# Kernel tuning notes

Hardware: AMD Instinct MI355X
Metric: run time of the kernel (lower is better)

The kernel has to match this reference:

```python
import jax, jax.numpy as jnp
import numpy as np

NUM_HEADS = 12
EMBED_DIM = 768
HEAD_DIM = EMBED_DIM // NUM_HEADS


def _rope_cos_sin():
    # Faithful to source: RoPE is applied with seq_dim=1 on [b,h,n,d] tensors,
    # so the "position" axis is actually the HEAD axis (length NUM_HEADS).
    inv_freq = 1.0 / (10000.0 ** (jnp.arange(0, HEAD_DIM, 2, dtype=jnp.float32) / HEAD_DIM))
    t = jnp.arange(NUM_HEADS, dtype=jnp.float32)
    freqs = t[:, None] * inv_freq[None, :]            # [H, D/2]
    emb = jnp.concatenate([freqs, freqs], axis=-1)     # [H, D]
    cos = jnp.cos(emb)[None, :, None, :]               # [1, H, 1, D] broadcasts over seq
    sin = jnp.sin(emb)[None, :, None, :]
    return cos, sin


def _apply_rope(x, cos, sin):
    # x: [B, H, N, D]
    x1, x2 = jnp.split(x, 2, axis=-1)
    x_rot = jnp.concatenate([-x2, x1], axis=-1)
    return x * cos + x_rot * sin


def setup_inputs() -> dict:
    key = jax.random.key(0)
    k1, k2, k3, k4, k5 = jax.random.split(key, 5)
    B, N, E = 8, 1024, EMBED_DIM
    s_in = 1.0 / np.sqrt(E)
    return {
        "x": jax.random.normal(k1, (B, N, E), dtype=jnp.float32),
        "w_qkv": jax.random.uniform(k2, (E, 3 * E), dtype=jnp.float32, minval=-s_in, maxval=s_in),
        "b_qkv": jax.random.uniform(k3, (3 * E,), dtype=jnp.float32, minval=-s_in, maxval=s_in),
        "w_proj": jax.random.uniform(k4, (E, E), dtype=jnp.float32, minval=-s_in, maxval=s_in),
        "b_proj": jax.random.uniform(k5, (E,), dtype=jnp.float32, minval=-s_in, maxval=s_in),
    }


def reference(x, w_qkv, b_qkv, w_proj, b_proj):
    B, N, E = x.shape
    H, D = NUM_HEADS, HEAD_DIM
    scale = D ** (-0.5)

    qkv = x @ w_qkv + b_qkv                                  # [B, N, 3E]
    qkv = qkv.reshape(B, N, 3, H, D).transpose(2, 0, 3, 1, 4)  # [3, B, H, N, D]
    q, k, v = qkv[0], qkv[1], qkv[2]

    cos, sin = _rope_cos_sin()
    q = _apply_rope(q, cos, sin)
    k = _apply_rope(k, cos, sin)

    attn = jnp.einsum('bhid,bhjd->bhij', q, k) * scale       # [B, H, N, N]
    attn = jax.nn.softmax(attn, axis=-1)
    out = jnp.einsum('bhij,bhjd->bhid', attn, v)             # [B, H, N, D]
    out = out.transpose(0, 2, 1, 3).reshape(B, N, E)         # [B, N, E]
    return out @ w_proj + b_proj
```

## Files before the change

kernel.cpp:

```cpp
#include <hip/hip_runtime.h>
#include <math.h>

#define NH 12
#define HD 64
#define NSEQ 1024
#define BATCH 8
#define EMB 768
#define NQKV 2304
#define MROWS 8192

typedef _Float16 half8 __attribute__((ext_vector_type(8)));
typedef _Float16 half4 __attribute__((ext_vector_type(4)));
typedef _Float16 half2v __attribute__((ext_vector_type(2)));
typedef float f32x4 __attribute__((ext_vector_type(4)));
typedef float f32x16 __attribute__((ext_vector_type(16)));
typedef unsigned int u32;

#define MFMA16(a,b,c) __builtin_amdgcn_mfma_f32_16x16x32_f16(a, b, c, 0, 0, 0)
#define MFMA32(a,b,c) __builtin_amdgcn_mfma_f32_32x32x16_f16(a, b, c, 0, 0, 0)

__device__ __forceinline__ void gld_lds16(const _Float16* g, _Float16* l) {
  __builtin_amdgcn_global_load_lds((const __attribute__((address_space(1))) u32*)g,
                                   (__attribute__((address_space(3))) u32*)l, 16, 0, 0);
}

__device__ __forceinline__ void transpose_tile(const float* __restrict__ in,
                                               _Float16* __restrict__ out,
                                               int R, int C, int bx, int by,
                                               _Float16 (*T)[72]) {
  const int tr = by * 64, tc = bx * 64;
  const int r = threadIdx.x >> 2, s = threadIdx.x & 3;
  const float* src = in + (size_t)(tr + r) * C + tc + s * 16;
  _Float16* dst = &T[r][s * 16];
  #pragma unroll
  for (int i = 0; i < 4; ++i) {
    float4 v = ((const float4*)src)[i];
    dst[4*i+0] = (_Float16)v.x; dst[4*i+1] = (_Float16)v.y;
    dst[4*i+2] = (_Float16)v.z; dst[4*i+3] = (_Float16)v.w;
  }
  __syncthreads();
  alignas(16) _Float16 tmp[16];
  #pragma unroll
  for (int j = 0; j < 16; ++j) tmp[j] = T[s * 16 + j][r];
  half8* o = (half8*)(out + (size_t)(tc + r) * R + tr + s * 16);
  o[0] = *(half8*)&tmp[0];
  o[1] = *(half8*)&tmp[8];
}

__global__ __launch_bounds__(256) void prepass(const float* __restrict__ x,
                                               _Float16* __restrict__ xh,
                                               const float* __restrict__ wq,
                                               _Float16* __restrict__ wqT,
                                               const float* __restrict__ wp,
                                               _Float16* __restrict__ wpT) {
  __shared__ _Float16 T[64][72];
  const int bid = blockIdx.x;
  if (bid < 6144) {
    int i = bid * 256 + threadIdx.x;
    float4 v = ((const float4*)x)[i];
    half4 h = { (_Float16)v.x, (_Float16)v.y, (_Float16)v.z, (_Float16)v.w };
    ((half4*)xh)[i] = h;
  } else if (bid < 6576) {
    int idx = bid - 6144;
    transpose_tile(wq, wqT, EMB, NQKV, idx % 36, idx / 36, T);
  } else {
    int idx = bid - 6576;
    transpose_tile(wp, wpT, EMB, EMB, idx % 12, idx / 12, T);
  }
}

template<int MODE>
__global__ __launch_bounds__(256) void gemm_mfma(const _Float16* __restrict__ A,
                                                 const _Float16* __restrict__ BT,
                                                 const float* __restrict__ bias,
                                                 float* __restrict__ outf,
                                                 _Float16* __restrict__ qo,
                                                 _Float16* __restrict__ ko,
                                                 _Float16* __restrict__ vo,
                                                 int K) {
  const int BUFH = 128 * 32;
  __shared__ __align__(16) _Float16 As[2 * 128 * 32];
  __shared__ __align__(16) _Float16 Bs[2 * 128 * 32];
  const int tid = threadIdx.x;
  const int lane = tid & 63, wave = tid >> 6;
  const int quad = lane >> 4, l15 = lane & 15;
  const int wm = (wave >> 1) * 64, wn = (wave & 1) * 64;
  const int row0 = blockIdx.y * 128, col0 = blockIdx.x * 128;

  const int srow = lane >> 2;
  const int sseg = (lane & 3) ^ ((srow >> 1) & 3);
  const _Float16* gA = A + (size_t)(row0 + wave*32 + srow) * K + sseg * 8;
  const _Float16* gB = BT + (size_t)(col0 + wave*32 + srow) * K + sseg * 8;
  _Float16* lA0 = As + (wave*32) * 32;
  _Float16* lA1 = As + (wave*32 + 16) * 32;
  _Float16* lB0 = Bs + (wave*32) * 32;
  _Float16* lB1 = Bs + (wave*32 + 16) * 32;

  const int xq = (quad ^ ((l15 >> 1) & 3)) * 8;

  f32x4 acc[4][4];
  #pragma unroll
  for (int i = 0; i < 4; ++i)
    #pragma unroll
    for (int j = 0; j < 4; ++j) {
      f32x4 z = {0.f, 0.f, 0.f, 0.f};
      acc[i][j] = z;
    }

  gld_lds16(gA,          lA0);
  gld_lds16(gA + 16 * K, lA1);
  gld_lds16(gB,          lB0);
  gld_lds16(gB + 16 * K, lB1);

  int buf = 0;
  for (int k0 = 0; k0 < K; k0 += 32, buf ^= 1) {
    __syncthreads();
    if (k0 + 32 < K) {
      const int nb = (buf ^ 1) * BUFH;
      gld_lds16(gA + k0 + 32,          lA0 + nb);
      gld_lds16(gA + k0 + 32 + 16 * K, lA1 + nb);
      gld_lds16(gB + k0 + 32,          lB0 + nb);
      gld_lds16(gB + k0 + 32 + 16 * K, lB1 + nb);
    }
    const _Float16* Ab = As + buf * BUFH;
    const _Float16* Bb = Bs + buf * BUFH;
    half8 af[4], bf[4];
    #pragma unroll
    for (int mt = 0; mt < 4; ++mt)
      af[mt] = *(const half8*)(Ab + (wm + mt*16 + l15) * 32 + xq);
    #pragma unroll
    for (int nt = 0; nt < 4; ++nt)
      bf[nt] = *(const half8*)(Bb + (wn + nt*16 + l15) * 32 + xq);
    #pragma unroll
    for (int mt = 0; mt < 4; ++mt)
      #pragma unroll
      for (int nt = 0; nt < 4; ++nt)
        acc[mt][nt] = MFMA16(af[mt], bf[nt], acc[mt][nt]);
  }

  float bcol[4];
  #pragma unroll
  for (int nt = 0; nt < 4; ++nt)
    bcol[nt] = bias[col0 + wn + nt*16 + l15];

  if (MODE == 0) {
    const int ch = col0 + wn;
    const int tt = ch / EMB;
    const int hh = (ch % EMB) >> 6;
    float cs[2], sn[2];
    if (tt < 2) {
      #pragma unroll
      for (int j = 0; j < 2; ++j) {
        float fi = (float)(j*16 + l15);
        float ang = (float)hh * expf(-0.28782313662425574f * fi);
        sincosf(ang, &sn[j], &cs[j]);
      }
    }
    #pragma unroll
    for (int mt = 0; mt < 4; ++mt) {
      int m0 = row0 + wm + mt*16 + quad*4;
      int b = m0 >> 10, n0 = m0 & 1023;
      size_t bh = (size_t)(b * NH + hh);
      if (tt == 2) {
        int np = (n0 & ~12) | ((n0 & 4) << 1) | ((n0 & 8) >> 1);
        #pragma unroll
        for (int nt = 0; nt < 4; ++nt) {
          int d = nt*16 + l15;
          half4 pk;
          #pragma unroll
          for (int r = 0; r < 4; ++r)
            pk[r] = (_Float16)(acc[mt][nt][r] + bcol[nt]);
          *(half4*)(vo + (bh * HD + d) * NSEQ + np) = pk;
        }
      } else {
        _Float16* dst = (tt == 0) ? qo : ko;
        const float sc = (tt == 0) ? 0.125f : 1.0f;
        #pragma unroll
        for (int j = 0; j < 2; ++j) {
          #pragma unroll
          for (int r = 0; r < 4; ++r) {
            float lo = acc[mt][j][r]     + bcol[j];
            float hi = acc[mt][j + 2][r] + bcol[j + 2];
            float nlo = (lo * cs[j] - hi * sn[j]) * sc;
            float nhi = (hi * cs[j] + lo * sn[j]) * sc;
            size_t rowoff = (bh * NSEQ + (size_t)(n0 + r)) * HD;
            dst[rowoff + j*16 + l15]      = (_Float16)nlo;
            dst[rowoff + j*16 + l15 + 32] = (_Float16)nhi;
          }
        }
      }
    }
  } else {
    #pragma unroll
    for (int mt = 0; mt < 4; ++mt) {
      int m0 = row0 + wm + mt*16 + quad*4;
      #pragma unroll
      for (int nt = 0; nt < 4; ++nt)
        #pragma unroll
        for (int r = 0; r < 4; ++r)
          outf[(size_t)(m0 + r) * EMB + col0 + wn + nt*16 + l15] =
              acc[mt][nt][r] + bcol[nt];
    }
  }
}

__global__ __launch_bounds__(256) void attn_mfma32(const _Float16* __restrict__ q,
                                                   const _Float16* __restrict__ k,
                                                   const _Float16* __restrict__ vt,
                                                   _Float16* __restrict__ ao) {
  const int BUFH = 64 * 64;
  __shared__ __align__(16) _Float16 Ks[2 * 64 * 64];
  __shared__ __align__(16) _Float16 Vs[2 * 64 * 64];
  const int tid = threadIdx.x;
  const int lane = tid & 63, wave = tid >> 6;
  const int l31 = lane & 31, hi = lane >> 5;
  const int bh = blockIdx.y;
  const int qrow = blockIdx.x * 128 + wave * 32 + l31;
  const size_t base = (size_t)bh * NSEQ * HD;

  const _Float16* qp = q + base + (size_t)qrow * HD + hi * 8;
  half8 qf[4];
  #pragma unroll
  for (int kh = 0; kh < 4; ++kh)
    qf[kh] = *(const half8*)(qp + kh * 16);

  const int srow = lane >> 3;
  const int sxor = (lane & 7) ^ (srow & 7);
  const _Float16* kg = k + base + (size_t)(wave*16 + srow) * HD + sxor * 8;
  const _Float16* vg = vt + (size_t)bh * HD * NSEQ
                       + (size_t)(wave*16 + srow) * NSEQ + sxor * 8;
  const int lofs = (wave * 16) * 64;

  int xofs[4];
  #pragma unroll
  for (int kh = 0; kh < 4; ++kh)
    xofs[kh] = ((kh*2 + hi) ^ (l31 & 7)) * 8;

  f32x16 O[2];
  #pragma unroll
  for (int dt = 0; dt < 2; ++dt)
    #pragma unroll
    for (int r = 0; r < 16; ++r) O[dt][r] = 0.f;
  float l = 0.f;

  gld_lds16(kg,             Ks + lofs);
  gld_lds16(kg + 8 * HD,    Ks + lofs + 8 * 64);
  gld_lds16(vg,             Vs + lofs);
  gld_lds16(vg + 8 * NSEQ,  Vs + lofs + 8 * 64);

  int buf = 0;
  for (int c0 = 0; c0 < NSEQ; c0 += 64, buf ^= 1) {
    __syncthreads();
    if (c0 + 64 < NSEQ) {
      const int nb = (buf ^ 1) * BUFH;
      gld_lds16(kg + (size_t)(c0 + 64) * HD,      Ks + nb + lofs);
      gld_lds16(kg + (size_t)(c0 + 72) * HD,      Ks + nb + lofs + 8 * 64);
      gld_lds16(vg + c0 + 64,                     Vs + nb + lofs);
      gld_lds16(vg + 8 * NSEQ + c0 + 64,          Vs + nb + lofs + 8 * 64);
    }
    const _Float16* Kb = Ks + buf * BUFH;
    const _Float16* Vb = Vs + buf * BUFH;

    f32x16 ct[2];
    #pragma unroll
    for (int kt = 0; kt < 2; ++kt) {
      #pragma unroll
      for (int r = 0; r < 16; ++r) ct[kt][r] = 0.f;
      #pragma unroll
      for (int kh = 0; kh < 4; ++kh) {
        half8 kf = *(const half8*)(Kb + (kt*32 + l31) * 64 + xofs[kh]);
        ct[kt] = MFMA32(kf, qf[kh], ct[kt]);
      }
    }

    union { half2v v; int i; } ph2[16];
    float rs = 0.f;
    #pragma unroll
    for (int kt = 0; kt < 2; ++kt)
      #pragma unroll
      for (int rp = 0; rp < 8; ++rp) {
        float p0 = __expf(ct[kt][2*rp]     - 4.0f);
        float p1 = __expf(ct[kt][2*rp + 1] - 4.0f);
        rs += p0 + p1;
        half2v hp = { (_Float16)p0, (_Float16)p1 };
        ph2[kt*8 + rp].v = hp;
      }
    l += rs;

    #pragma unroll
    for (int kh = 0; kh < 4; ++kh) {
      const int kt = kh >> 1;
      const int iA = kt*8 + (kh & 1)*4;
      union { half8 h; int d[4]; } pf;
      pf.d[0] = ph2[iA].i;     pf.d[1] = ph2[iA + 1].i;
      pf.d[2] = ph2[iA + 2].i; pf.d[3] = ph2[iA + 3].i;
      #pragma unroll
      for (int dt = 0; dt < 2; ++dt) {
        half8 vf = *(const half8*)(Vb + (dt*32 + l31) * 64 + xofs[kh]);
        O[dt] = MFMA32(vf, pf.h, O[dt]);
      }
    }
  }

  l += __shfl_xor(l, 32);

  const int b = bh / NH, hh = bh % NH;
  const float inv = 1.0f / l;
  _Float16* orow = ao + (size_t)(b * NSEQ + qrow) * EMB + hh * HD;
  #pragma unroll
  for (int dt = 0; dt < 2; ++dt)
    #pragma unroll
    for (int t = 0; t < 4; ++t) {
      int d0 = dt*32 + 8*t + 4*hi;
      half4 o4;
      #pragma unroll
      for (int j = 0; j < 4; ++j)
        o4[j] = (_Float16)(O[dt][4*t + j] * inv);
      *(half4*)(orow + d0) = o4;
    }
}

extern "C" void kernel_launch(void* const* d_in, const int* in_sizes, int n_in,
                              void* d_out, int out_size, void* d_ws, size_t ws_size,
                              hipStream_t stream) {
  const float* x      = (const float*)d_in[0];
  const float* w_qkv  = (const float*)d_in[1];
  const float* b_qkv  = (const float*)d_in[2];
  const float* w_proj = (const float*)d_in[3];
  const float* b_proj = (const float*)d_in[4];
  float* out = (float*)d_out;

  _Float16* xh  = (_Float16*)d_ws;
  _Float16* wqT = xh  + (size_t)MROWS * EMB;
  _Float16* wpT = wqT + (size_t)NQKV * EMB;
  _Float16* qh  = wpT + (size_t)EMB * EMB;
  _Float16* kh  = qh  + (size_t)BATCH*NH*NSEQ*HD;
  _Float16* vth = kh  + (size_t)BATCH*NH*NSEQ*HD;
  _Float16* aoh = vth + (size_t)BATCH*NH*NSEQ*HD;

  prepass<<<6720, 256, 0, stream>>>(x, xh, w_qkv, wqT, w_proj, wpT);

  gemm_mfma<0><<<dim3(NQKV/128, MROWS/128), 256, 0, stream>>>(
      xh, wqT, b_qkv, nullptr, qh, kh, vth, EMB);

  attn_mfma32<<<dim3(NSEQ/128, BATCH*NH), 256, 0, stream>>>(qh, kh, vth, aoh);

  gemm_mfma<1><<<dim3(EMB/128, MROWS/128), 256, 0, stream>>>(
      aoh, wpT, b_proj, out, nullptr, nullptr, nullptr, EMB);
}
```

Measured before the change: 205.7 us.

## Replace direct global-to-LDS loads with register-staged double-buffered prefetch

Both the GEMM and the attention kernel stop using global_load_lds and instead load the next tile into registers at the start of each iteration, compute on the current LDS buffer, then write the registers into the other LDS buffer before one barrier. The swizzle moves from the global address to the LDS write address. The aim is to hide global latency behind the MFMA work and to move the barrier to the end of the loop. In exchange it adds VGPR pressure and separate ds_write instructions, which can lower occupancy.

Measured after the change: 201.9 us. About the same (-1.9%).

```diff
diff --git a/kernel.cpp b/kernel.cpp
--- a/kernel.cpp
+++ b/kernel.cpp
@@ -18,11 +18,6 @@
 
 #define MFMA16(a,b,c) __builtin_amdgcn_mfma_f32_16x16x32_f16(a, b, c, 0, 0, 0)
 #define MFMA32(a,b,c) __builtin_amdgcn_mfma_f32_32x32x16_f16(a, b, c, 0, 0, 0)
-
-__device__ __forceinline__ void gld_lds16(const _Float16* g, _Float16* l) {
-  __builtin_amdgcn_global_load_lds((const __attribute__((address_space(1))) u32*)g,
-                                   (__attribute__((address_space(3))) u32*)l, 16, 0, 0);
-}
 
 __device__ __forceinline__ void transpose_tile(const float* __restrict__ in,
                                                _Float16* __restrict__ out,
@@ -88,13 +83,12 @@
   const int row0 = blockIdx.y * 128, col0 = blockIdx.x * 128;
 
   const int srow = lane >> 2;
-  const int sseg = (lane & 3) ^ ((srow >> 1) & 3);
+  const int sseg = lane & 3;
+  const int wseg = sseg ^ ((srow >> 1) & 3);
   const _Float16* gA = A + (size_t)(row0 + wave*32 + srow) * K + sseg * 8;
   const _Float16* gB = BT + (size_t)(col0 + wave*32 + srow) * K + sseg * 8;
-  _Float16* lA0 = As + (wave*32) * 32;
-  _Float16* lA1 = As + (wave*32 + 16) * 32;
-  _Float16* lB0 = Bs + (wave*32) * 32;
-  _Float16* lB1 = Bs + (wave*32 + 16) * 32;
+  _Float16* wA0 = As + (wave*32 + srow) * 32 + wseg * 8;
+  _Float16* wB0 = Bs + (wave*32 + srow) * 32 + wseg * 8;
 
   const int xq = (quad ^ ((l15 >> 1) & 3)) * 8;
 
@@ -107,20 +101,24 @@
       acc[i][j] = z;
     }
 
-  gld_lds16(gA,          lA0);
-  gld_lds16(gA + 16 * K, lA1);
-  gld_lds16(gB,          lB0);
-  gld_lds16(gB + 16 * K, lB1);
+  half8 ra0 = *(const half8*)(gA);
+  half8 ra1 = *(const half8*)(gA + 16 * K);
+  half8 rb0 = *(const half8*)(gB);
+  half8 rb1 = *(const half8*)(gB + 16 * K);
+  *(half8*)(wA0)          = ra0;
+  *(half8*)(wA0 + 16*32)  = ra1;
+  *(half8*)(wB0)          = rb0;
+  *(half8*)(wB0 + 16*32)  = rb1;
+  __syncthreads();
 
   int buf = 0;
-  for (int k0 = 0; k0 < K; k0 += 32, buf ^= 1) {
-    __syncthreads();
-    if (k0 + 32 < K) {
-      const int nb = (buf ^ 1) * BUFH;
-      gld_lds16(gA + k0 + 32,          lA0 + nb);
-      gld_lds16(gA + k0 + 32 + 16 * K, lA1 + nb);
-      gld_lds16(gB + k0 + 32,          lB0 + nb);
-      gld_lds16(gB + k0 + 32 + 16 * K, lB1 + nb);
+  for (int k0 = 0; k0 < K; k0 += 32) {
+    const bool more = (k0 + 32 < K);
+    if (more) {
+      ra0 = *(const half8*)(gA + k0 + 32);
+      ra1 = *(const half8*)(gA + k0 + 32 + 16 * K);
+      rb0 = *(const half8*)(gB + k0 + 32);
+      rb1 = *(const half8*)(gB + k0 + 32 + 16 * K);
     }
     const _Float16* Ab = As + buf * BUFH;
     const _Float16* Bb = Bs + buf * BUFH;
@@ -136,6 +134,15 @@
       #pragma unroll
       for (int nt = 0; nt < 4; ++nt)
         acc[mt][nt] = MFMA16(af[mt], bf[nt], acc[mt][nt]);
+    if (more) {
+      const int nb = (buf ^ 1) * BUFH;
+      *(half8*)(wA0 + nb)         = ra0;
+      *(half8*)(wA0 + nb + 16*32) = ra1;
+      *(half8*)(wB0 + nb)         = rb0;
+      *(half8*)(wB0 + nb + 16*32) = rb1;
+    }
+    __syncthreads();
+    buf ^= 1;
   }
 
   float bcol[4];
@@ -224,12 +231,14 @@
   for (int kh = 0; kh < 4; ++kh)
     qf[kh] = *(const half8*)(qp + kh * 16);
 
-  const int srow = lane >> 3;
-  const int sxor = (lane & 7) ^ (srow & 7);
-  const _Float16* kg = k + base + (size_t)(wave*16 + srow) * HD + sxor * 8;
+  const int srow8 = lane >> 3;
+  const int sseg8 = lane & 7;
+  const int wseg8 = sseg8 ^ (srow8 & 7);
+  const _Float16* kg = k + base + (size_t)(wave*16 + srow8) * HD + sseg8 * 8;
   const _Float16* vg = vt + (size_t)bh * HD * NSEQ
-                       + (size_t)(wave*16 + srow) * NSEQ + sxor * 8;
-  const int lofs = (wave * 16) * 64;
+                       + (size_t)(wave*16 + srow8) * NSEQ + sseg8 * 8;
+  _Float16* wK0 = Ks + (wave*16 + srow8) * 64 + wseg8 * 8;
+  _Float16* wV0 = Vs + (wave*16 + srow8) * 64 + wseg8 * 8;
 
   int xofs[4];
   #pragma unroll
@@ -243,20 +252,24 @@
     for (int r = 0; r < 16; ++r) O[dt][r] = 0.f;
   float l = 0.f;
 
-  gld_lds16(kg,             Ks + lofs);
-  gld_lds16(kg + 8 * HD,    Ks + lofs + 8 * 64);
-  gld_lds16(vg,             Vs + lofs);
-  gld_lds16(vg + 8 * NSEQ,  Vs + lofs + 8 * 64);
+  half8 rk0 = *(const half8*)(kg);
+  half8 rk1 = *(const half8*)(kg + 8 * HD);
+  half8 rv0 = *(const half8*)(vg);
+  half8 rv1 = *(const half8*)(vg + 8 * NSEQ);
+  *(half8*)(wK0)          = rk0;
+  *(half8*)(wK0 + 8*64)   = rk1;
+  *(half8*)(wV0)          = rv0;
+  *(half8*)(wV0 + 8*64)   = rv1;
+  __syncthreads();
 
   int buf = 0;
-  for (int c0 = 0; c0 < NSEQ; c0 += 64, buf ^= 1) {
-    __syncthreads();
-    if (c0 + 64 < NSEQ) {
-      const int nb = (buf ^ 1) * BUFH;
-      gld_lds16(kg + (size_t)(c0 + 64) * HD,      Ks + nb + lofs);
-      gld_lds16(kg + (size_t)(c0 + 72) * HD,      Ks + nb + lofs + 8 * 64);
-      gld_lds16(vg + c0 + 64,                     Vs + nb + lofs);
-      gld_lds16(vg + 8 * NSEQ + c0 + 64,          Vs + nb + lofs + 8 * 64);
+  for (int c0 = 0; c0 < NSEQ; c0 += 64) {
+    const bool more = (c0 + 64 < NSEQ);
+    if (more) {
+      rk0 = *(const half8*)(kg + (size_t)(c0 + 64) * HD);
+      rk1 = *(const half8*)(kg + (size_t)(c0 + 72) * HD);
+      rv0 = *(const half8*)(vg + c0 + 64);
+      rv1 = *(const half8*)(vg + 8 * NSEQ + c0 + 64);
     }
     const _Float16* Kb = Ks + buf * BUFH;
     const _Float16* Vb = Vs + buf * BUFH;
@@ -300,6 +313,16 @@
         O[dt] = MFMA32(vf, pf.h, O[dt]);
       }
     }
+
+    if (more) {
+      const int nb = (buf ^ 1) * BUFH;
+      *(half8*)(wK0 + nb)        = rk0;
+      *(half8*)(wK0 + nb + 8*64) = rk1;
+      *(half8*)(wV0 + nb)        = rv0;
+      *(half8*)(wV0 + nb + 8*64) = rv1;
+    }
+    __syncthreads();
+    buf ^= 1;
   }
 
   l += __shfl_xor(l, 32);
```
